# Performance work log

Measured on AMD Instinct MI355X. Metric: run time of the kernel, lower is better.

Reference implementation:

```python
import jax, jax.numpy as jnp
import numpy as np
from jax import lax

# Paraformer-large streaming decoder dims
L, H, DFF, NH, DK, K, V, T, S, CKV, LB = 16, 512, 2048, 4, 128, 11, 8404, 64, 2048, 256, 256


def _ln(x, g, b, eps=1e-5):
    m = jnp.mean(x, axis=-1, keepdims=True)
    var = jnp.mean((x - m) ** 2, axis=-1, keepdims=True)
    return (x - m) * lax.rsqrt(var + eps) * g + b


def setup_inputs() -> dict:
    key = jax.random.key(0)
    ks = jax.random.split(key, 20)
    w = lambda k, shp: jax.random.normal(k, shp, jnp.float32) * 0.02
    return {
        "encoder_out": jax.random.normal(ks[0], (1, S, H), jnp.float32),
        "list_frame": jax.random.normal(ks[1], (1, T, H), jnp.float32),
        "fsmn_cache": jax.random.normal(ks[2], (L, 1, H, K - 1), jnp.float32),
        "key_cache": jax.random.normal(ks[3], (L, NH, DK, CKV), jnp.float32),
        "value_cache": jax.random.normal(ks[4], (L, NH, CKV, DK), jnp.float32),
        "norm1_g": jnp.ones((L, H)), "norm1_b": jnp.zeros((L, H)),
        "norm2_g": jnp.ones((L, H)), "norm2_b": jnp.zeros((L, H)),
        "norm3_g": jnp.ones((L, H)), "norm3_b": jnp.zeros((L, H)),
        "ffn_norm_g": jnp.ones((L, DFF)), "ffn_norm_b": jnp.zeros((L, DFF)),
        "w1": w(ks[5], (L, H, DFF)), "b1": jnp.zeros((L, DFF)),
        "w2": w(ks[6], (L, DFF, H)),  # bias-free in FunASR DecoderSANM
        "fsmn_w": w(ks[7], (L, H, K)),  # depthwise conv, groups=H, no bias
        "qw": w(ks[8], (L, H, H)), "qb": jnp.zeros((L, H)),
        "kvw": w(ks[9], (L, H, 2 * H)), "kvb": jnp.zeros((L, 2 * H)),
        "ow": w(ks[10], (L, H, H)), "ob": jnp.zeros((L, H)),
        "d3_norm1_g": jnp.ones((H,)), "d3_norm1_b": jnp.zeros((H,)),
        "d3_w1": w(ks[11], (H, DFF)), "d3_b1": jnp.zeros((DFF,)),
        "d3_ffn_norm_g": jnp.ones((DFF,)), "d3_ffn_norm_b": jnp.zeros((DFF,)),
        "d3_w2": w(ks[12], (DFF, H)),
        "after_norm_g": jnp.ones((H,)), "after_norm_b": jnp.zeros((H,)),
        "out_w": w(ks[13], (H, V)), "out_b": jnp.zeros((V,)),
        "list_frame_len": T,
    }


def reference(encoder_out, list_frame, fsmn_cache, key_cache, value_cache,
              norm1_g, norm1_b, norm2_g, norm2_b, norm3_g, norm3_b,
              ffn_norm_g, ffn_norm_b, w1, b1, w2, fsmn_w, qw, qb, kvw, kvb, ow, ob,
              d3_norm1_g, d3_norm1_b, d3_w1, d3_b1, d3_ffn_norm_g, d3_ffn_norm_b, d3_w2,
              after_norm_g, after_norm_b, out_w, out_b, list_frame_len):
    enc = encoder_out[0]  # [S, H]
    scale = DK ** -0.5

    def layer_fn(lf, p):
        (fc, kc, vc, n1g, n1b, n2g, n2b, n3g, n3b, fng, fnb,
         W1, B1, W2, FW, QW, QB, KVW, KVB, OW, OB) = p
        residual = lf
        y = _ln(lf, n1g, n1b)
        y = _ln(jax.nn.relu(y @ W1 + B1), fng, fnb) @ W2
        y = _ln(y, n2g, n2b)
        # cache concat; slice [look_back:] with look_back = -(K-1)-T keeps all K-1+T cols
        x_cat = jnp.concatenate([fc, jnp.swapaxes(y, 1, 2)], axis=-1)  # [1, H, K-1+T]
        conv = lax.conv_general_dilated(
            x_cat, FW[:, None, :], (1,), 'VALID',
            dimension_numbers=('NCH', 'OIH', 'NCH'), feature_group_count=H)  # [1, H, T]
        x = jnp.swapaxes(conv, 1, 2) + y + residual
        residual = x
        q = (_ln(x, n3g, n3b)[0] @ QW + QB).reshape(-1, NH, DK).transpose(1, 0, 2) * scale  # [h, T, dk]
        kv = enc @ KVW + KVB  # [S, 2H]
        k = kv[:, :H].reshape(-1, NH, DK).transpose(1, 2, 0)  # [h, dk, S]
        v = kv[:, H:].reshape(-1, NH, DK).transpose(1, 0, 2)  # [h, S, dk]
        k = jnp.concatenate([kc, k], axis=2)  # [h, dk, CKV+S]
        v = jnp.concatenate([vc, v], axis=1)  # [h, CKV+S, dk]
        attn = jax.nn.softmax(jnp.einsum('htd,hds->hts', q, k), axis=-1)
        ctx = jnp.einsum('hts,hsd->htd', attn, v).transpose(1, 0, 2).reshape(1, -1, H)
        lf = residual + ctx @ OW + OB
        return lf, (x_cat, k[:, :, -LB:], v[:, -LB:, :])

    layer_params = (fsmn_cache, key_cache, value_cache, norm1_g, norm1_b, norm2_g, norm2_b,
                    norm3_g, norm3_b, ffn_norm_g, ffn_norm_b, w1, b1, w2, fsmn_w,
                    qw, qb, kvw, kvb, ow, ob)
    lf, (save_fsmn, save_keys, save_values) = lax.scan(layer_fn, list_frame, layer_params)
    x = _ln(lf, d3_norm1_g, d3_norm1_b)
    x = _ln(jax.nn.relu(x @ d3_w1 + d3_b1), d3_ffn_norm_g, d3_ffn_norm_b) @ d3_w2
    logits = _ln(x, after_norm_g, after_norm_b) @ out_w + out_b
    max_logit_ids = jnp.argmax(logits, axis=-1).astype(jnp.int32)
    return save_fsmn, save_keys, save_values, max_logit_ids
```

## Files before the change

kernel.cpp:

```cpp
#include <hip/hip_runtime.h>

constexpr int LAY = 16, HID = 512, FF = 2048, NHD = 4, DKH = 128, KW = 11,
              VOC = 8404, TT = 64, SEQ = 2048, LBN = 256;

__global__ void diag_k(float* __restrict__ p, float v) { p[threadIdx.x] = v; }

__global__ __launch_bounds__(256) void redln_k(
    const float* __restrict__ P, int N, int nch,
    const float* __restrict__ bias, const float* __restrict__ res, int relu,
    const float* __restrict__ g, const float* __restrict__ b,
    float* __restrict__ out1, float* __restrict__ out2) {
  __shared__ float buf[2048];
  __shared__ float red[256];
  const int m = blockIdx.x, tid = threadIdx.x;
  float s = 0.f;
  for (int n = tid; n < N; n += 256) {
    const float* p = P + (size_t)m * N + n;
    float v = 0.f;
    for (int c = 0; c < nch; ++c) v += p[(size_t)c * 64 * N];
    if (bias) v += bias[n];
    if (res) v += res[(size_t)m * N + n];
    if (relu) v = fmaxf(v, 0.f);
    if (out1) out1[(size_t)m * N + n] = v;
    buf[n] = v; s += v;
  }
  red[tid] = s; __syncthreads();
  for (int st = 128; st > 0; st >>= 1) { if (tid < st) red[tid] += red[tid + st]; __syncthreads(); }
  const float mean = red[0] / N;
  __syncthreads();
  float vs = 0.f;
  for (int n = tid; n < N; n += 256) { float d = buf[n] - mean; vs += d * d; }
  red[tid] = vs; __syncthreads();
  for (int st = 128; st > 0; st >>= 1) { if (tid < st) red[tid] += red[tid + st]; __syncthreads(); }
  const float inv = rsqrtf(red[0] / N + 1e-5f);
  for (int n = tid; n < N; n += 256)
    out2[(size_t)m * N + n] = (buf[n] - mean) * inv * g[n] + b[n];
}

__global__ __launch_bounds__(256) void gemm_nn(
    const float* __restrict__ A, int lda, long sA,
    const float* __restrict__ B, int ldb, long sB,
    float* __restrict__ C, int ldc, long sC,
    const float* __restrict__ bias,
    const float* __restrict__ res, int ldres,
    int N, int Kd, int flags, int nch,
    float* __restrict__ part, long pzs, int coff,
    int aCh, long aChS) {
  __shared__ float As[64][68];
  __shared__ float Bs[64][68];
  const int tid = threadIdx.x;
  const int lr = tid >> 4, lc = tid & 15;
  const int bn = blockIdx.x * 64;
  const int chunk = blockIdx.y;
  const int z = blockIdx.z;
  A += (long)z * sA; B += (long)z * sB; C += (long)z * sC;
  float acc[4][4] = {};
  const int ktiles = Kd >> 6;
  for (int kt = chunk; kt < ktiles; kt += nch) {
    const int k0 = kt << 6;
    __syncthreads();
#pragma unroll
    for (int i = 0; i < 4; ++i) {
      const int r = lr + 16 * i;
      const float* ap = A + (size_t)r * lda + k0 + lc * 4;
      float4 av = *(const float4*)ap;
      for (int c = 1; c < aCh; ++c) {
        const float4 t2 = *(const float4*)(ap + (size_t)c * aChS);
        av.x += t2.x; av.y += t2.y; av.z += t2.z; av.w += t2.w;
      }
      As[lc * 4 + 0][r] = av.x; As[lc * 4 + 1][r] = av.y;
      As[lc * 4 + 2][r] = av.z; As[lc * 4 + 3][r] = av.w;
      const int n = bn + lc * 4;
      const float* bp = B + (size_t)(k0 + r) * ldb + n;
      float4 bv;
      if (n + 3 < N) bv = *(const float4*)bp;
      else {
        bv.x = (n + 0 < N) ? bp[0] : 0.f;
        bv.y = (n + 1 < N) ? bp[1] : 0.f;
        bv.z = (n + 2 < N) ? bp[2] : 0.f;
        bv.w = (n + 3 < N) ? bp[3] : 0.f;
      }
      *(float4*)(&Bs[r][lc * 4]) = bv;
    }
    __syncthreads();
#pragma unroll 8
    for (int kk = 0; kk < 64; ++kk) {
      const float4 a = *(const float4*)(&As[kk][lr * 4]);
      const float4 b = *(const float4*)(&Bs[kk][lc * 4]);
      acc[0][0] += a.x * b.x; acc[0][1] += a.x * b.y; acc[0][2] += a.x * b.z; acc[0][3] += a.x * b.w;
      acc[1][0] += a.y * b.x; acc[1][1] += a.y * b.y; acc[1][2] += a.y * b.z; acc[1][3] += a.y * b.w;
      acc[2][0] += a.z * b.x; acc[2][1] += a.z * b.y; acc[2][2] += a.z * b.z; acc[2][3] += a.z * b.w;
      acc[3][0] += a.w * b.x; acc[3][1] += a.w * b.y; acc[3][2] += a.w * b.z; acc[3][3] += a.w * b.w;
    }
  }
  if (part) {
    float* P = part + (size_t)z * pzs + (size_t)(coff + chunk) * 64 * N;
#pragma unroll
    for (int i = 0; i < 4; ++i) {
      const int m = lr * 4 + i;
#pragma unroll
      for (int j = 0; j < 4; ++j) P[(size_t)m * N + bn + lc * 4 + j] = acc[i][j];
    }
    return;
  }
#pragma unroll
  for (int i = 0; i < 4; ++i) {
    const int m = lr * 4 + i;
#pragma unroll
    for (int j = 0; j < 4; ++j) {
      const int n = bn + lc * 4 + j;
      if (n < N) {
        float v = acc[i][j];
        if (bias) v += bias[n];
        if (res) v += res[(size_t)m * ldres + n];
        if (flags & 2) v += C[(size_t)m * ldc + n];
        if (flags & 1) v = fmaxf(v, 0.f);
        C[(size_t)m * ldc + n] = v;
      }
    }
  }
}

__global__ __launch_bounds__(256) void red_k(
    const float* __restrict__ P, float* __restrict__ out,
    int N, int nch, long pzs, int outld, int zoff,
    const float* __restrict__ bias, const float* __restrict__ res,
    const float* __restrict__ rsv, const float* __restrict__ bvv,
    int relu, int total) {
  const int idx = blockIdx.x * 256 + threadIdx.x;
  if (idx >= total) return;
  const int z = idx / (64 * N);
  const int rem = idx - z * 64 * N;
  const int t = rem / N;
  const int n = rem - t * N;
  const float* p = P + (size_t)z * pzs + (size_t)t * N + n;
  float s = 0.f;
  for (int c = 0; c < nch; ++c) s += p[(size_t)c * 64 * N];
  const int oc = z * zoff + n;
  if (bias) s += bias[oc];
  if (res) s += res[(size_t)t * outld + oc];
  if (rsv) s += rsv[z * 64 + t] * bvv[oc];
  if (relu) s = fmaxf(s, 0.f);
  out[(size_t)t * outld + oc] = s;
}

__global__ __launch_bounds__(256) void gemm_nt(
    const float* __restrict__ A, int lda, long sA,
    const float* __restrict__ B, int ldb, long sB,
    float* __restrict__ C, int ldc, long sC,
    int N, int Kd) {
  __shared__ float As[64][68];
  __shared__ float Bs[64][68];
  const int tid = threadIdx.x;
  const int lr = tid >> 4, lc = tid & 15;
  const int bn = blockIdx.x * 64;
  const int z = blockIdx.z;
  A += (long)z * sA; B += (long)z * sB; C += (long)z * sC;
  float acc[4][4] = {};
  for (int k0 = 0; k0 < Kd; k0 += 64) {
    __syncthreads();
#pragma unroll
    for (int i = 0; i < 4; ++i) {
      const int r = lr + 16 * i;
      const float4 av = *(const float4*)(A + (size_t)r * lda + k0 + lc * 4);
      As[lc * 4 + 0][r] = av.x; As[lc * 4 + 1][r] = av.y;
      As[lc * 4 + 2][r] = av.z; As[lc * 4 + 3][r] = av.w;
      const float4 bv = *(const float4*)(B + (size_t)(bn + r) * ldb + k0 + lc * 4);
      Bs[lc * 4 + 0][r] = bv.x; Bs[lc * 4 + 1][r] = bv.y;
      Bs[lc * 4 + 2][r] = bv.z; Bs[lc * 4 + 3][r] = bv.w;
    }
    __syncthreads();
#pragma unroll 8
    for (int kk = 0; kk < 64; ++kk) {
      const float4 a = *(const float4*)(&As[kk][lr * 4]);
      const float4 b = *(const float4*)(&Bs[kk][lc * 4]);
      acc[0][0] += a.x * b.x; acc[0][1] += a.x * b.y; acc[0][2] += a.x * b.z; acc[0][3] += a.x * b.w;
      acc[1][0] += a.y * b.x; acc[1][1] += a.y * b.y; acc[1][2] += a.y * b.z; acc[1][3] += a.y * b.w;
      acc[2][0] += a.z * b.x; acc[2][1] += a.z * b.y; acc[2][2] += a.z * b.z; acc[2][3] += a.z * b.w;
      acc[3][0] += a.w * b.x; acc[3][1] += a.w * b.y; acc[3][2] += a.w * b.z; acc[3][3] += a.w * b.w;
    }
  }
#pragma unroll
  for (int i = 0; i < 4; ++i) {
    const int m = lr * 4 + i;
#pragma unroll
    for (int j = 0; j < 4; ++j) {
      const int n = bn + lc * 4 + j;
      C[(size_t)m * ldc + n] = acc[i][j];
    }
  }
}

__global__ __launch_bounds__(256) void attn1_k(
    const float* __restrict__ qbf, const float* __restrict__ Wkv,
    const float* __restrict__ kcl,
    float* __restrict__ qp, float* __restrict__ sc,
    int ckv, int sct) {
  __shared__ float As[64][68];
  __shared__ float Bs[64][68];
  const int tid = threadIdx.x;
  const int lr = tid >> 4, lc = tid & 15;
  const int h = blockIdx.z;
  const bool isQp = blockIdx.x < 8;
  const int bn = (isQp ? blockIdx.x : blockIdx.x - 8) * 64;
  const float* A = qbf + h * DKH;
  float acc[4][4] = {};
  for (int k0 = 0; k0 < DKH; k0 += 64) {
    __syncthreads();
#pragma unroll
    for (int i = 0; i < 4; ++i) {
      const int r = lr + 16 * i;
      const float4 av = *(const float4*)(A + (size_t)r * HID + k0 + lc * 4);
      As[lc * 4 + 0][r] = av.x; As[lc * 4 + 1][r] = av.y;
      As[lc * 4 + 2][r] = av.z; As[lc * 4 + 3][r] = av.w;
      if (isQp) {
        const float4 bv = *(const float4*)(Wkv + (size_t)(bn + r) * (2 * HID) + h * DKH + k0 + lc * 4);
        Bs[lc * 4 + 0][r] = bv.x; Bs[lc * 4 + 1][r] = bv.y;
        Bs[lc * 4 + 2][r] = bv.z; Bs[lc * 4 + 3][r] = bv.w;
      } else {
        const float4 bv = *(const float4*)(kcl + ((size_t)h * DKH + k0 + r) * ckv + bn + lc * 4);
        *(float4*)(&Bs[r][lc * 4]) = bv;
      }
    }
    __syncthreads();
#pragma unroll 8
    for (int kk = 0; kk < 64; ++kk) {
      const float4 a = *(const float4*)(&As[kk][lr * 4]);
      const float4 b = *(const float4*)(&Bs[kk][lc * 4]);
      acc[0][0] += a.x * b.x; acc[0][1] += a.x * b.y; acc[0][2] += a.x * b.z; acc[0][3] += a.x * b.w;
      acc[1][0] += a.y * b.x; acc[1][1] += a.y * b.y; acc[1][2] += a.y * b.z; acc[1][3] += a.y * b.w;
      acc[2][0] += a.z * b.x; acc[2][1] += a.z * b.y; acc[2][2] += a.z * b.z; acc[2][3] += a.z * b.w;
      acc[3][0] += a.w * b.x; acc[3][1] += a.w * b.y; acc[3][2] += a.w * b.z; acc[3][3] += a.w * b.w;
    }
  }
  if (isQp) {
    float* C = qp + (size_t)h * TT * HID;
#pragma unroll
    for (int i = 0; i < 4; ++i)
#pragma unroll
      for (int j = 0; j < 4; ++j)
        C[(size_t)(lr * 4 + i) * HID + bn + lc * 4 + j] = acc[i][j];
  } else {
    float* C = sc + (size_t)h * TT * sct;
#pragma unroll
    for (int i = 0; i < 4; ++i)
#pragma unroll
      for (int j = 0; j < 4; ++j)
        C[(size_t)(lr * 4 + i) * sct + bn + lc * 4 + j] = acc[i][j];
  }
}

__global__ __launch_bounds__(256) void attn2_k(
    const float* __restrict__ sc, const float* __restrict__ vcl,
    const float* __restrict__ enc,
    float* __restrict__ part, float* __restrict__ partE,
    int ckv, int sct, int ncho, long pzc) {
  __shared__ float As[64][68];
  __shared__ float Bs[64][68];
  const int tid = threadIdx.x;
  const int lr = tid >> 4, lc = tid & 15;
  const int h = blockIdx.z;
  const int by = blockIdx.y;
  const bool isOld = blockIdx.x < 2;
  if (isOld && by >= ncho) return;
  if (!isOld && by >= 4) return;
  const float* A;
  const float* Bb;
  int lda, ldb, N, ktiles, nch, bn;
  float* P;
  if (isOld) {
    A = sc + (size_t)h * TT * sct;  lda = sct;
    Bb = vcl + (size_t)h * ckv * DKH; ldb = DKH;
    N = DKH; ktiles = ckv >> 6; nch = ncho; bn = blockIdx.x * 64;
    P = part + (size_t)h * pzc + (size_t)by * 64 * DKH;
  } else {
    A = sc + ckv + (size_t)h * TT * sct; lda = sct;
    Bb = enc; ldb = HID;
    N = HID; ktiles = SEQ >> 6; nch = 4; bn = (blockIdx.x - 2) * 64;
    P = partE + (size_t)h * (4L * 64 * HID) + (size_t)by * 64 * HID;
  }
  float acc[4][4] = {};
  for (int kt = by; kt < ktiles; kt += nch) {
    const int k0 = kt << 6;
    __syncthreads();
#pragma unroll
    for (int i = 0; i < 4; ++i) {
      const int r = lr + 16 * i;
      const float4 av = *(const float4*)(A + (size_t)r * lda + k0 + lc * 4);
      As[lc * 4 + 0][r] = av.x; As[lc * 4 + 1][r] = av.y;
      As[lc * 4 + 2][r] = av.z; As[lc * 4 + 3][r] = av.w;
      const float4 bv = *(const float4*)(Bb + (size_t)(k0 + r) * ldb + bn + lc * 4);
      *(float4*)(&Bs[r][lc * 4]) = bv;
    }
    __syncthreads();
#pragma unroll 8
    for (int kk = 0; kk < 64; ++kk) {
      const float4 a = *(const float4*)(&As[kk][lr * 4]);
      const float4 b = *(const float4*)(&Bs[kk][lc * 4]);
      acc[0][0] += a.x * b.x; acc[0][1] += a.x * b.y; acc[0][2] += a.x * b.z; acc[0][3] += a.x * b.w;
      acc[1][0] += a.y * b.x; acc[1][1] += a.y * b.y; acc[1][2] += a.y * b.z; acc[1][3] += a.y * b.w;
      acc[2][0] += a.z * b.x; acc[2][1] += a.z * b.y; acc[2][2] += a.z * b.z; acc[2][3] += a.z * b.w;
      acc[3][0] += a.w * b.x; acc[3][1] += a.w * b.y; acc[3][2] += a.w * b.z; acc[3][3] += a.w * b.w;
    }
  }
#pragma unroll
  for (int i = 0; i < 4; ++i)
#pragma unroll
    for (int j = 0; j < 4; ++j)
      P[(size_t)(lr * 4 + i) * N + bn + lc * 4 + j] = acc[i][j];
}

__global__ __launch_bounds__(128) void fsmn_k(const float* __restrict__ y4,
                                              const float* __restrict__ lfin,
                                              const float* __restrict__ cache,
                                              const float* __restrict__ fw,
                                              float* __restrict__ xout,
                                              float* __restrict__ xcat_out) {
  __shared__ float xc[KW - 1 + TT];
  const int tid = threadIdx.x, h = blockIdx.x;
  if (tid < KW - 1) xc[tid] = cache[h * (KW - 1) + tid];
  else if (tid < KW - 1 + TT) xc[tid] = y4[(size_t)(tid - (KW - 1)) * HID + h];
  __syncthreads();
  if (tid < KW - 1 + TT) xcat_out[h * (KW - 1 + TT) + tid] = xc[tid];
  if (tid < TT) {
    float a = 0.f;
#pragma unroll
    for (int k = 0; k < KW; ++k) a += xc[tid + k] * fw[h * KW + k];
    const size_t o = (size_t)tid * HID + h;
    xout[o] = a + y4[o] + lfin[o];
  }
}

__global__ __launch_bounds__(256) void softmax_k(float* __restrict__ sc,
                                                 float* __restrict__ rs,
                                                 const float* __restrict__ qbf,
                                                 const float* __restrict__ kb,
                                                 int cols, int newStart, float alpha) {
  __shared__ float red[256];
  const int tid = threadIdx.x;
  const int row = blockIdx.x;
  const int h = row >> 6, t = row & 63;
  sc += (size_t)row * cols;
  float qv = 0.f;
  if (tid < DKH) qv = qbf[t * HID + h * DKH + tid] * kb[h * DKH + tid];
  red[tid] = qv; __syncthreads();
  for (int st = 64; st > 0; st >>= 1) { if (tid < st) red[tid] += red[tid + st]; __syncthreads(); }
  const float qcv = red[0];
  __syncthreads();
  float m = -3.4e38f;
  for (int c = tid; c < cols; c += 256) {
    float v = (sc[c] + (c >= newStart ? qcv : 0.f)) * alpha;
    m = fmaxf(m, v);
  }
  red[tid] = m; __syncthreads();
  for (int st = 128; st > 0; st >>= 1) { if (tid < st) red[tid] = fmaxf(red[tid], red[tid + st]); __syncthreads(); }
  m = red[0]; __syncthreads();
  float s = 0.f;
  for (int c = tid; c < cols; c += 256) {
    float v = (sc[c] + (c >= newStart ? qcv : 0.f)) * alpha;
    float e = __expf(v - m);
    sc[c] = e; s += e;
  }
  red[tid] = s; __syncthreads();
  for (int st = 128; st > 0; st >>= 1) { if (tid < st) red[tid] += red[tid + st]; __syncthreads(); }
  const float inv = 1.f / red[0];
  float ns = 0.f;
  for (int c = tid; c < cols; c += 256) {
    float p = sc[c] * inv; sc[c] = p;
    if (c >= newStart) ns += p;
  }
  __syncthreads();
  red[tid] = ns; __syncthreads();
  for (int st = 128; st > 0; st >>= 1) { if (tid < st) red[tid] += red[tid + st]; __syncthreads(); }
  if (tid == 0) rs[row] = red[0];
}

__global__ __launch_bounds__(256) void argmax_k(const float* __restrict__ lg,
                                                float* __restrict__ out) {
  __shared__ float vs[256];
  __shared__ int ix[256];
  const int tid = threadIdx.x;
  lg += (size_t)blockIdx.x * VOC;
  float bm = -3.4e38f;
  int bi = 0;
  for (int c = tid; c < VOC; c += 256) { float v = lg[c]; if (v > bm) { bm = v; bi = c; } }
  vs[tid] = bm; ix[tid] = bi; __syncthreads();
  for (int st = 128; st > 0; st >>= 1) {
    if (tid < st) {
      if (vs[tid + st] > vs[tid] || (vs[tid + st] == vs[tid] && ix[tid + st] < ix[tid])) {
        vs[tid] = vs[tid + st]; ix[tid] = ix[tid + st];
      }
    }
    __syncthreads();
  }
  if (tid == 0) out[blockIdx.x] = (float)ix[0];
}

__global__ __launch_bounds__(256) void kvsave_k(const float* __restrict__ enc,
                                                const float* __restrict__ kvw,
                                                const float* __restrict__ kvb,
                                                float* __restrict__ keys,
                                                float* __restrict__ vals) {
  __shared__ float As[64][68];
  __shared__ float Bs[64][68];
  const int tid = threadIdx.x;
  const int lr = tid >> 4, lc = tid & 15;
  const int bn = blockIdx.x * 64, bm = blockIdx.y * 64;
  const int l = blockIdx.z;
  const float* W = kvw + (size_t)l * HID * 2 * HID;
  float acc[4][4] = {};
  for (int k0 = 0; k0 < HID; k0 += 64) {
    __syncthreads();
#pragma unroll
    for (int i = 0; i < 4; ++i) {
      const int r = lr + 16 * i;
      const float4 av =
          *(const float4*)(enc + (size_t)(SEQ - LBN + bm + r) * HID + k0 + lc * 4);
      As[lc * 4 + 0][r] = av.x; As[lc * 4 + 1][r] = av.y;
      As[lc * 4 + 2][r] = av.z; As[lc * 4 + 3][r] = av.w;
      const float4 bv = *(const float4*)(W + (size_t)(k0 + r) * (2 * HID) + bn + lc * 4);
      *(float4*)(&Bs[r][lc * 4]) = bv;
    }
    __syncthreads();
#pragma unroll 8
    for (int kk = 0; kk < 64; ++kk) {
      const float4 a = *(const float4*)(&As[kk][lr * 4]);
      const float4 b = *(const float4*)(&Bs[kk][lc * 4]);
      acc[0][0] += a.x * b.x; acc[0][1] += a.x * b.y; acc[0][2] += a.x * b.z; acc[0][3] += a.x * b.w;
      acc[1][0] += a.y * b.x; acc[1][1] += a.y * b.y; acc[1][2] += a.y * b.z; acc[1][3] += a.y * b.w;
      acc[2][0] += a.z * b.x; acc[2][1] += a.z * b.y; acc[2][2] += a.z * b.z; acc[2][3] += a.z * b.w;
      acc[3][0] += a.w * b.x; acc[3][1] += a.w * b.y; acc[3][2] += a.w * b.z; acc[3][3] += a.w * b.w;
    }
  }
#pragma unroll
  for (int i = 0; i < 4; ++i) {
    const int m = bm + lr * 4 + i;
#pragma unroll
    for (int j = 0; j < 4; ++j) {
      const int n = bn + lc * 4 + j;
      const float v = acc[i][j] + kvb[(size_t)l * 2 * HID + n];
      if (n < 512) {
        const int h = n >> 7, d = n & 127;
        keys[(((size_t)l * NHD + h) * DKH + d) * LBN + m] = v;
      } else {
        const int c = n - 512, h = c >> 7, d = c & 127;
        vals[(((size_t)l * NHD + h) * LBN + m) * DKH + d] = v;
      }
    }
  }
}

extern "C" void kernel_launch(void* const* d_in, const int* in_sizes, int n_in,
                              void* d_out, int out_size, void* d_ws, size_t ws_size,
                              hipStream_t stream) {
  static const int EXPECT[34] = {
      1048576, 32768, 81920, -1, -1,
      8192, 8192, 8192, 8192, 8192, 8192,
      32768, 32768,
      16777216, 32768, 16777216, 90112,
      4194304, 8192, 8388608, 16384, 4194304, 8192,
      512, 512, 1048576, 2048, 2048, 2048, 1048576,
      512, 512, 4302848, 8404};
  if (out_size != 4800576) {
    diag_k<<<1, 64, 0, stream>>>((float*)d_out, 9800000.f);
    return;
  }
  float* out_fsmn = (float*)d_out;
  float* out_keys = out_fsmn + (size_t)LAY * HID * (KW - 1 + TT);
  float* out_vals = out_keys + (size_t)LAY * NHD * DKH * LBN;
  float* out_ids  = out_vals + (size_t)LAY * NHD * LBN * DKH;
  if (n_in < 34) {
    diag_k<<<1, 64, 0, stream>>>(out_ids, 9900000.f);
    return;
  }
  for (int i = 0; i < 34; ++i) {
    if (EXPECT[i] >= 0 && in_sizes[i] != EXPECT[i]) {
      diag_k<<<1, 64, 0, stream>>>(out_ids, (float)((i + 1) * 100000));
      return;
    }
  }
  const long per = (long)LAY * NHD * DKH;
  const long ckl = (long)in_sizes[3] / per;
  if ((long)in_sizes[3] != ckl * per || in_sizes[4] != in_sizes[3] ||
      ckl <= 0 || (ckl & 63) != 0 || ckl > 6144) {
    diag_k<<<1, 64, 0, stream>>>(out_fsmn, (float)in_sizes[3]);
    return;
  }
  const int ckv = (int)ckl;
  const int sct = ckv + SEQ;
  const long TS = (long)TT * sct;
  const int ncho = (ckv / 64 < 8) ? (ckv / 64) : 8;

  const float* enc    = (const float*)d_in[0];
  const float* lfrm   = (const float*)d_in[1];
  const float* fcache = (const float*)d_in[2];
  const float* kcache = (const float*)d_in[3];
  const float* vcache = (const float*)d_in[4];
  const float* n1g = (const float*)d_in[5];  const float* n1b = (const float*)d_in[6];
  const float* n2g = (const float*)d_in[7];  const float* n2b = (const float*)d_in[8];
  const float* n3g = (const float*)d_in[9];  const float* n3b = (const float*)d_in[10];
  const float* fng = (const float*)d_in[11]; const float* fnb = (const float*)d_in[12];
  const float* w1  = (const float*)d_in[13]; const float* b1  = (const float*)d_in[14];
  const float* w2  = (const float*)d_in[15];
  const float* fw  = (const float*)d_in[16];
  const float* qw  = (const float*)d_in[17]; const float* qbi  = (const float*)d_in[18];
  const float* kvw = (const float*)d_in[19]; const float* kvbi = (const float*)d_in[20];
  const float* ow  = (const float*)d_in[21]; const float* obi  = (const float*)d_in[22];
  const float* d3n1g = (const float*)d_in[23]; const float* d3n1b = (const float*)d_in[24];
  const float* d3w1  = (const float*)d_in[25]; const float* d3b1  = (const float*)d_in[26];
  const float* d3fng = (const float*)d_in[27]; const float* d3fnb = (const float*)d_in[28];
  const float* d3w2  = (const float*)d_in[29];
  const float* ang   = (const float*)d_in[30]; const float* anb = (const float*)d_in[31];
  const float* outw  = (const float*)d_in[32]; const float* outb = (const float*)d_in[33];

  float* sc  = out_keys;
  float* ov  = out_vals;
  float* lf  = ov + 0;
  float* y1  = ov + 32768;
  float* y4  = ov + 98304;
  float* xb  = ov + 131072;
  float* qbf = ov + 163840;
  float* ctx = ov + 196608;
  float* y2  = ov + 360448;
  float* qp  = ov + 491520;
  float* rs  = ov + 753920;
  float* lg  = ov + 754176;
  float* partE = lg;
  float* part  = ov + 1292032;

  const float alpha = 0.08838834764831845f;
  const long TH = (long)TT * HID;
  const long pz_ctx = (long)(ncho + 4) * 64 * DKH;

  redln_k<<<TT, 256, 0, stream>>>(lfrm, HID, 1, nullptr, nullptr, 0,
                                  n1g, n1b, lf, y1);

  for (int l = 0; l < LAY; ++l) {
    const float* Wkv = kvw + (size_t)l * HID * 2 * HID;
    const float* Bkv = kvbi + (size_t)l * 2 * HID;
    gemm_nn<<<dim3(32, 4, 1), 256, 0, stream>>>(
        y1, HID, 0, w1 + (size_t)l * HID * FF, FF, 0, nullptr, 0, 0,
        nullptr, nullptr, 0, FF, HID, 0, 4, part, 0, 0, 1, 0);
    redln_k<<<TT, 256, 0, stream>>>(part, FF, 4, b1 + (size_t)l * FF, nullptr, 1,
                                    fng + (size_t)l * FF, fnb + (size_t)l * FF,
                                    nullptr, y2);
    gemm_nn<<<dim3(8, 16, 1), 256, 0, stream>>>(
        y2, FF, 0, w2 + (size_t)l * FF * HID, HID, 0, nullptr, 0, 0,
        nullptr, nullptr, 0, HID, FF, 0, 16, part, 0, 0, 1, 0);
    redln_k<<<TT, 256, 0, stream>>>(part, HID, 16, nullptr, nullptr, 0,
                                    n2g + l * HID, n2b + l * HID, nullptr, y4);
    fsmn_k<<<HID, 128, 0, stream>>>(y4, lf, fcache + (size_t)l * HID * (KW - 1),
                                    fw + (size_t)l * HID * KW, xb,
                                    out_fsmn + (size_t)l * HID * (KW - 1 + TT));
    redln_k<<<TT, 256, 0, stream>>>(xb, HID, 1, nullptr, nullptr, 0,
                                    n3g + l * HID, n3b + l * HID, nullptr, y1);
    gemm_nn<<<dim3(8, 8, 1), 256, 0, stream>>>(
        y1, HID, 0, qw + (size_t)l * HID * HID, HID, 0, nullptr, 0, 0,
        nullptr, nullptr, 0, HID, HID, 0, 8, part, 0, 0, 1, 0);
    red_k<<<128, 256, 0, stream>>>(part, qbf, HID, 8, 0, HID, HID,
                                   qbi + (size_t)l * HID, nullptr, nullptr, nullptr,
                                   0, TT * HID);
    attn1_k<<<dim3(8 + ckv / 64, 1, NHD), 256, 0, stream>>>(
        qbf, Wkv, kcache + (size_t)l * NHD * DKH * ckv, qp, sc, ckv, sct);
    gemm_nt<<<dim3(32, 1, NHD), 256, 0, stream>>>(
        qp, HID, TH, enc, HID, 0, sc + ckv, sct, TS, SEQ, HID);
    softmax_k<<<NHD * TT, 256, 0, stream>>>(sc, rs, qbf, Bkv, sct, ckv, alpha);
    attn2_k<<<dim3(10, (ncho > 4 ? ncho : 4), NHD), 256, 0, stream>>>(
        sc, vcache + (size_t)l * NHD * ckv * DKH, enc, part, partE,
        ckv, sct, ncho, pz_ctx);
    gemm_nn<<<dim3(2, 4, NHD), 256, 0, stream>>>(
        partE, HID, 4L * 64 * HID, Wkv + HID, 2 * HID, DKH, nullptr, 0, 0,
        nullptr, nullptr, 0, DKH, HID, 0, 4, part, pz_ctx, ncho, 4, 64L * HID);
    red_k<<<128, 256, 0, stream>>>(part, ctx, DKH, ncho + 4, pz_ctx, HID, DKH,
                                   nullptr, nullptr, rs, Bkv + HID, 0, NHD * TT * DKH);
    gemm_nn<<<dim3(8, 8, 1), 256, 0, stream>>>(
        ctx, HID, 0, ow + (size_t)l * HID * HID, HID, 0, nullptr, 0, 0,
        nullptr, nullptr, 0, HID, HID, 0, 8, part, 0, 0, 1, 0);
    const float* ng = (l + 1 < LAY) ? n1g + (l + 1) * HID : d3n1g;
    const float* nb = (l + 1 < LAY) ? n1b + (l + 1) * HID : d3n1b;
    redln_k<<<TT, 256, 0, stream>>>(part, HID, 8, obi + (size_t)l * HID, xb, 0,
                                    ng, nb, lf, y1);
  }

  gemm_nn<<<dim3(32, 4, 1), 256, 0, stream>>>(
      y1, HID, 0, d3w1, FF, 0, nullptr, 0, 0, nullptr, nullptr, 0,
      FF, HID, 0, 4, part, 0, 0, 1, 0);
  redln_k<<<TT, 256, 0, stream>>>(part, FF, 4, d3b1, nullptr, 1,
                                  d3fng, d3fnb, nullptr, y2);
  gemm_nn<<<dim3(8, 16, 1), 256, 0, stream>>>(
      y2, FF, 0, d3w2, HID, 0, nullptr, 0, 0, nullptr, nullptr, 0,
      HID, FF, 0, 16, part, 0, 0, 1, 0);
  redln_k<<<TT, 256, 0, stream>>>(part, HID, 16, nullptr, nullptr, 0,
                                  ang, anb, nullptr, y4);
  gemm_nn<<<dim3((VOC + 63) / 64, 1, 1), 256, 0, stream>>>(
      y4, HID, 0, outw, VOC, 0, lg, VOC, 0, outb, nullptr, 0,
      VOC, HID, 0, 1, nullptr, 0, 0, 1, 0);
  argmax_k<<<TT, 256, 0, stream>>>(lg, out_ids);

  kvsave_k<<<dim3(2 * HID / 64, LBN / 64, LAY), 256, 0, stream>>>(
      enc, kvw, kvbi, out_keys, out_vals);
}
```

Baseline: 2.985 ms.

## Swizzle shared tiles, raise split-K, fuse FSMN+LN and q reduction into consumers

Replaces padded 64x68 shared tiles with XOR-swizzled 64x64 layouts across all GEMM kernels to avoid bank conflicts. Doubles split-K chunk counts for FFN and attention GEMMs and adds split-K to gemm_nt, with partials moved to the workspace. Fuses the FSMN conv with the following LayerNorm, and folds the q-projection partial reduction into attn1 and softmax, removing a red_k launch. Softmax caches its row in shared memory so it no longer rereads global scores. More partial chunks add reduction traffic, and a workspace-size check is added.

```diff
diff --git a/kernel.cpp b/kernel.cpp
--- a/kernel.cpp
+++ b/kernel.cpp
@@ -2,6 +2,8 @@
 
 constexpr int LAY = 16, HID = 512, FF = 2048, NHD = 4, DKH = 128, KW = 11,
               VOC = 8404, TT = 64, SEQ = 2048, LBN = 256;
+
+#define SWZ(row, e) ((e) ^ ((((row) >> 2) & 7) << 2))
 
 __global__ void diag_k(float* __restrict__ p, float v) { p[threadIdx.x] = v; }
 
@@ -46,8 +48,8 @@
     int N, int Kd, int flags, int nch,
     float* __restrict__ part, long pzs, int coff,
     int aCh, long aChS) {
-  __shared__ float As[64][68];
-  __shared__ float Bs[64][68];
+  __shared__ float As[64][64];
+  __shared__ float Bs[64][64];
   const int tid = threadIdx.x;
   const int lr = tid >> 4, lc = tid & 15;
   const int bn = blockIdx.x * 64;
@@ -56,6 +58,7 @@
   A += (long)z * sA; B += (long)z * sB; C += (long)z * sC;
   float acc[4][4] = {};
   const int ktiles = Kd >> 6;
+  const int fa = (lc & 7) << 2;
   for (int kt = chunk; kt < ktiles; kt += nch) {
     const int k0 = kt << 6;
     __syncthreads();
@@ -68,8 +71,8 @@
         const float4 t2 = *(const float4*)(ap + (size_t)c * aChS);
         av.x += t2.x; av.y += t2.y; av.z += t2.z; av.w += t2.w;
       }
-      As[lc * 4 + 0][r] = av.x; As[lc * 4 + 1][r] = av.y;
-      As[lc * 4 + 2][r] = av.z; As[lc * 4 + 3][r] = av.w;
+      As[lc * 4 + 0][r ^ fa] = av.x; As[lc * 4 + 1][r ^ fa] = av.y;
+      As[lc * 4 + 2][r ^ fa] = av.z; As[lc * 4 + 3][r ^ fa] = av.w;
       const int n = bn + lc * 4;
       const float* bp = B + (size_t)(k0 + r) * ldb + n;
       float4 bv;
@@ -80,13 +83,14 @@
         bv.z = (n + 2 < N) ? bp[2] : 0.f;
         bv.w = (n + 3 < N) ? bp[3] : 0.f;
       }
-      *(float4*)(&Bs[r][lc * 4]) = bv;
+      *(float4*)(&Bs[r][SWZ(r, lc * 4)]) = bv;
     }
     __syncthreads();
 #pragma unroll 8
     for (int kk = 0; kk < 64; ++kk) {
-      const float4 a = *(const float4*)(&As[kk][lr * 4]);
-      const float4 b = *(const float4*)(&Bs[kk][lc * 4]);
+      const int fk = ((kk >> 2) & 7) << 2;
+      const float4 a = *(const float4*)(&As[kk][(lr * 4) ^ fk]);
+      const float4 b = *(const float4*)(&Bs[kk][(lc * 4) ^ fk]);
       acc[0][0] += a.x * b.x; acc[0][1] += a.x * b.y; acc[0][2] += a.x * b.z; acc[0][3] += a.x * b.w;
       acc[1][0] += a.y * b.x; acc[1][1] += a.y * b.y; acc[1][2] += a.y * b.z; acc[1][3] += a.y * b.w;
       acc[2][0] += a.z * b.x; acc[2][1] += a.z * b.y; acc[2][2] += a.z * b.z; acc[2][3] += a.z * b.w;
@@ -148,85 +152,103 @@
     const float* __restrict__ A, int lda, long sA,
     const float* __restrict__ B, int ldb, long sB,
     float* __restrict__ C, int ldc, long sC,
-    int N, int Kd) {
-  __shared__ float As[64][68];
-  __shared__ float Bs[64][68];
+    int N, int Kd, int nch, float* __restrict__ part) {
+  __shared__ float As[64][64];
+  __shared__ float Bs[64][64];
   const int tid = threadIdx.x;
   const int lr = tid >> 4, lc = tid & 15;
   const int bn = blockIdx.x * 64;
+  const int chunk = blockIdx.y;
   const int z = blockIdx.z;
   A += (long)z * sA; B += (long)z * sB; C += (long)z * sC;
   float acc[4][4] = {};
-  for (int k0 = 0; k0 < Kd; k0 += 64) {
+  const int ktiles = Kd >> 6;
+  const int fa = (lc & 7) << 2;
+  for (int kt = chunk; kt < ktiles; kt += nch) {
+    const int k0 = kt << 6;
     __syncthreads();
 #pragma unroll
     for (int i = 0; i < 4; ++i) {
       const int r = lr + 16 * i;
       const float4 av = *(const float4*)(A + (size_t)r * lda + k0 + lc * 4);
-      As[lc * 4 + 0][r] = av.x; As[lc * 4 + 1][r] = av.y;
-      As[lc * 4 + 2][r] = av.z; As[lc * 4 + 3][r] = av.w;
+      As[lc * 4 + 0][r ^ fa] = av.x; As[lc * 4 + 1][r ^ fa] = av.y;
+      As[lc * 4 + 2][r ^ fa] = av.z; As[lc * 4 + 3][r ^ fa] = av.w;
       const float4 bv = *(const float4*)(B + (size_t)(bn + r) * ldb + k0 + lc * 4);
-      Bs[lc * 4 + 0][r] = bv.x; Bs[lc * 4 + 1][r] = bv.y;
-      Bs[lc * 4 + 2][r] = bv.z; Bs[lc * 4 + 3][r] = bv.w;
+      Bs[lc * 4 + 0][r ^ fa] = bv.x; Bs[lc * 4 + 1][r ^ fa] = bv.y;
+      Bs[lc * 4 + 2][r ^ fa] = bv.z; Bs[lc * 4 + 3][r ^ fa] = bv.w;
     }
     __syncthreads();
 #pragma unroll 8
     for (int kk = 0; kk < 64; ++kk) {
-      const float4 a = *(const float4*)(&As[kk][lr * 4]);
-      const float4 b = *(const float4*)(&Bs[kk][lc * 4]);
+      const int fk = ((kk >> 2) & 7) << 2;
+      const float4 a = *(const float4*)(&As[kk][(lr * 4) ^ fk]);
+      const float4 b = *(const float4*)(&Bs[kk][(lc * 4) ^ fk]);
       acc[0][0] += a.x * b.x; acc[0][1] += a.x * b.y; acc[0][2] += a.x * b.z; acc[0][3] += a.x * b.w;
       acc[1][0] += a.y * b.x; acc[1][1] += a.y * b.y; acc[1][2] += a.y * b.z; acc[1][3] += a.y * b.w;
       acc[2][0] += a.z * b.x; acc[2][1] += a.z * b.y; acc[2][2] += a.z * b.z; acc[2][3] += a.z * b.w;
       acc[3][0] += a.w * b.x; acc[3][1] += a.w * b.y; acc[3][2] += a.w * b.z; acc[3][3] += a.w * b.w;
     }
   }
-#pragma unroll
-  for (int i = 0; i < 4; ++i) {
-    const int m = lr * 4 + i;
-#pragma unroll
-    for (int j = 0; j < 4; ++j) {
-      const int n = bn + lc * 4 + j;
-      C[(size_t)m * ldc + n] = acc[i][j];
-    }
+  if (chunk == 0) {
+#pragma unroll
+    for (int i = 0; i < 4; ++i)
+#pragma unroll
+      for (int j = 0; j < 4; ++j)
+        C[(size_t)(lr * 4 + i) * ldc + bn + lc * 4 + j] = acc[i][j];
+  } else {
+    float* P = part + (size_t)z * (64L * SEQ) + (size_t)(chunk - 1) * 64 * SEQ * NHD;
+#pragma unroll
+    for (int i = 0; i < 4; ++i)
+#pragma unroll
+      for (int j = 0; j < 4; ++j)
+        P[(size_t)(lr * 4 + i) * SEQ + bn + lc * 4 + j] = acc[i][j];
   }
 }
 
 __global__ __launch_bounds__(256) void attn1_k(
-    const float* __restrict__ qbf, const float* __restrict__ Wkv,
-    const float* __restrict__ kcl,
+    const float* __restrict__ qpart, const float* __restrict__ qbi_l,
+    const float* __restrict__ Wkv, const float* __restrict__ kcl,
     float* __restrict__ qp, float* __restrict__ sc,
     int ckv, int sct) {
-  __shared__ float As[64][68];
-  __shared__ float Bs[64][68];
+  __shared__ float As[64][64];
+  __shared__ float Bs[64][64];
   const int tid = threadIdx.x;
   const int lr = tid >> 4, lc = tid & 15;
   const int h = blockIdx.z;
   const bool isQp = blockIdx.x < 8;
   const int bn = (isQp ? blockIdx.x : blockIdx.x - 8) * 64;
-  const float* A = qbf + h * DKH;
+  const int fa = (lc & 7) << 2;
   float acc[4][4] = {};
   for (int k0 = 0; k0 < DKH; k0 += 64) {
     __syncthreads();
 #pragma unroll
     for (int i = 0; i < 4; ++i) {
       const int r = lr + 16 * i;
-      const float4 av = *(const float4*)(A + (size_t)r * HID + k0 + lc * 4);
-      As[lc * 4 + 0][r] = av.x; As[lc * 4 + 1][r] = av.y;
-      As[lc * 4 + 2][r] = av.z; As[lc * 4 + 3][r] = av.w;
+      const float* ap = qpart + (size_t)r * HID + h * DKH + k0 + lc * 4;
+      float4 av = *(const float4*)ap;
+      for (int c = 1; c < 8; ++c) {
+        const float4 t2 = *(const float4*)(ap + (size_t)c * 64 * HID);
+        av.x += t2.x; av.y += t2.y; av.z += t2.z; av.w += t2.w;
+      }
+      const float4 bb = *(const float4*)(qbi_l + h * DKH + k0 + lc * 4);
+      av.x += bb.x; av.y += bb.y; av.z += bb.z; av.w += bb.w;
+      As[lc * 4 + 0][r ^ fa] = av.x; As[lc * 4 + 1][r ^ fa] = av.y;
+      As[lc * 4 + 2][r ^ fa] = av.z; As[lc * 4 + 3][r ^ fa] = av.w;
       if (isQp) {
         const float4 bv = *(const float4*)(Wkv + (size_t)(bn + r) * (2 * HID) + h * DKH + k0 + lc * 4);
-        Bs[lc * 4 + 0][r] = bv.x; Bs[lc * 4 + 1][r] = bv.y;
-        Bs[lc * 4 + 2][r] = bv.z; Bs[lc * 4 + 3][r] = bv.w;
+        Bs[lc * 4 + 0][r ^ fa] = bv.x; Bs[lc * 4 + 1][r ^ fa] = bv.y;
+        Bs[lc * 4 + 2][r ^ fa] = bv.z; Bs[lc * 4 + 3][r ^ fa] = bv.w;
       } else {
         const float4 bv = *(const float4*)(kcl + ((size_t)h * DKH + k0 + r) * ckv + bn + lc * 4);
-        *(float4*)(&Bs[r][lc * 4]) = bv;
+        *(float4*)(&Bs[r][SWZ(r, lc * 4)]) = bv;
       }
     }
     __syncthreads();
 #pragma unroll 8
     for (int kk = 0; kk < 64; ++kk) {
-      const float4 a = *(const float4*)(&As[kk][lr * 4]);
-      const float4 b = *(const float4*)(&Bs[kk][lc * 4]);
+      const int fk = ((kk >> 2) & 7) << 2;
+      const float4 a = *(const float4*)(&As[kk][(lr * 4) ^ fk]);
+      const float4 b = *(const float4*)(&Bs[kk][(lc * 4) ^ fk]);
       acc[0][0] += a.x * b.x; acc[0][1] += a.x * b.y; acc[0][2] += a.x * b.z; acc[0][3] += a.x * b.w;
       acc[1][0] += a.y * b.x; acc[1][1] += a.y * b.y; acc[1][2] += a.y * b.z; acc[1][3] += a.y * b.w;
       acc[2][0] += a.z * b.x; acc[2][1] += a.z * b.y; acc[2][2] += a.z * b.z; acc[2][3] += a.z * b.w;
@@ -255,15 +277,15 @@
     const float* __restrict__ enc,
     float* __restrict__ part, float* __restrict__ partE,
     int ckv, int sct, int ncho, long pzc) {
-  __shared__ float As[64][68];
-  __shared__ float Bs[64][68];
+  __shared__ float As[64][64];
+  __shared__ float Bs[64][64];
   const int tid = threadIdx.x;
   const int lr = tid >> 4, lc = tid & 15;
   const int h = blockIdx.z;
   const int by = blockIdx.y;
   const bool isOld = blockIdx.x < 2;
   if (isOld && by >= ncho) return;
-  if (!isOld && by >= 4) return;
+  if (!isOld && by >= 8) return;
   const float* A;
   const float* Bb;
   int lda, ldb, N, ktiles, nch, bn;
@@ -276,9 +298,10 @@
   } else {
     A = sc + ckv + (size_t)h * TT * sct; lda = sct;
     Bb = enc; ldb = HID;
-    N = HID; ktiles = SEQ >> 6; nch = 4; bn = (blockIdx.x - 2) * 64;
-    P = partE + (size_t)h * (4L * 64 * HID) + (size_t)by * 64 * HID;
-  }
+    N = HID; ktiles = SEQ >> 6; nch = 8; bn = (blockIdx.x - 2) * 64;
+    P = partE + (size_t)h * (8L * 64 * HID) + (size_t)by * 64 * HID;
+  }
+  const int fa = (lc & 7) << 2;
   float acc[4][4] = {};
   for (int kt = by; kt < ktiles; kt += nch) {
     const int k0 = kt << 6;
@@ -287,16 +310,17 @@
     for (int i = 0; i < 4; ++i) {
       const int r = lr + 16 * i;
       const float4 av = *(const float4*)(A + (size_t)r * lda + k0 + lc * 4);
-      As[lc * 4 + 0][r] = av.x; As[lc * 4 + 1][r] = av.y;
-      As[lc * 4 + 2][r] = av.z; As[lc * 4 + 3][r] = av.w;
+      As[lc * 4 + 0][r ^ fa] = av.x; As[lc * 4 + 1][r ^ fa] = av.y;
+      As[lc * 4 + 2][r ^ fa] = av.z; As[lc * 4 + 3][r ^ fa] = av.w;
       const float4 bv = *(const float4*)(Bb + (size_t)(k0 + r) * ldb + bn + lc * 4);
-      *(float4*)(&Bs[r][lc * 4]) = bv;
+      *(float4*)(&Bs[r][SWZ(r, lc * 4)]) = bv;
     }
     __syncthreads();
 #pragma unroll 8
     for (int kk = 0; kk < 64; ++kk) {
-      const float4 a = *(const float4*)(&As[kk][lr * 4]);
-      const float4 b = *(const float4*)(&Bs[kk][lc * 4]);
+      const int fk = ((kk >> 2) & 7) << 2;
+      const float4 a = *(const float4*)(&As[kk][(lr * 4) ^ fk]);
+      const float4 b = *(const float4*)(&Bs[kk][(lc * 4) ^ fk]);
       acc[0][0] += a.x * b.x; acc[0][1] += a.x * b.y; acc[0][2] += a.x * b.z; acc[0][3] += a.x * b.w;
       acc[1][0] += a.y * b.x; acc[1][1] += a.y * b.y; acc[1][2] += a.y * b.z; acc[1][3] += a.y * b.w;
       acc[2][0] += a.z * b.x; acc[2][1] += a.z * b.y; acc[2][2] += a.z * b.z; acc[2][3] += a.z * b.w;
@@ -310,63 +334,93 @@
       P[(size_t)(lr * 4 + i) * N + bn + lc * 4 + j] = acc[i][j];
 }
 
-__global__ __launch_bounds__(128) void fsmn_k(const float* __restrict__ y4,
-                                              const float* __restrict__ lfin,
-                                              const float* __restrict__ cache,
-                                              const float* __restrict__ fw,
-                                              float* __restrict__ xout,
-                                              float* __restrict__ xcat_out) {
-  __shared__ float xc[KW - 1 + TT];
-  const int tid = threadIdx.x, h = blockIdx.x;
-  if (tid < KW - 1) xc[tid] = cache[h * (KW - 1) + tid];
-  else if (tid < KW - 1 + TT) xc[tid] = y4[(size_t)(tid - (KW - 1)) * HID + h];
+__global__ __launch_bounds__(256) void fsmnln_k(
+    const float* __restrict__ y4, const float* __restrict__ lfin,
+    const float* __restrict__ cache, const float* __restrict__ fw,
+    const float* __restrict__ g, const float* __restrict__ b,
+    float* __restrict__ xb, float* __restrict__ xcat,
+    float* __restrict__ y1out) {
+  __shared__ float buf[HID];
+  __shared__ float red[256];
+  const int t = blockIdx.x, tid = threadIdx.x;
+  float s = 0.f;
+  for (int h = tid; h < HID; h += 256) {
+    float conv = 0.f;
+#pragma unroll
+    for (int k = 0; k < KW; ++k) {
+      const int j = t + k;
+      const float xcv = (j < KW - 1) ? cache[h * (KW - 1) + j]
+                                     : y4[(size_t)(j - (KW - 1)) * HID + h];
+      conv += xcv * fw[h * KW + k];
+    }
+    const float yv = y4[(size_t)t * HID + h];
+    const float x = conv + yv + lfin[(size_t)t * HID + h];
+    xb[(size_t)t * HID + h] = x;
+    buf[h] = x; s += x;
+    xcat[h * (KW - 1 + TT) + (KW - 1) + t] = yv;
+    if (t == 0) {
+      for (int j2 = 0; j2 < KW - 1; ++j2)
+        xcat[h * (KW - 1 + TT) + j2] = cache[h * (KW - 1) + j2];
+    }
+  }
+  red[tid] = s; __syncthreads();
+  for (int st = 128; st > 0; st >>= 1) { if (tid < st) red[tid] += red[tid + st]; __syncthreads(); }
+  const float mean = red[0] / HID;
   __syncthreads();
-  if (tid < KW - 1 + TT) xcat_out[h * (KW - 1 + TT) + tid] = xc[tid];
-  if (tid < TT) {
-    float a = 0.f;
-#pragma unroll
-    for (int k = 0; k < KW; ++k) a += xc[tid + k] * fw[h * KW + k];
-    const size_t o = (size_t)tid * HID + h;
-    xout[o] = a + y4[o] + lfin[o];
-  }
-}
-
-__global__ __launch_bounds__(256) void softmax_k(float* __restrict__ sc,
-                                                 float* __restrict__ rs,
-                                                 const float* __restrict__ qbf,
-                                                 const float* __restrict__ kb,
-                                                 int cols, int newStart, float alpha) {
+  float vs = 0.f;
+  for (int h = tid; h < HID; h += 256) { float d = buf[h] - mean; vs += d * d; }
+  red[tid] = vs; __syncthreads();
+  for (int st = 128; st > 0; st >>= 1) { if (tid < st) red[tid] += red[tid + st]; __syncthreads(); }
+  const float inv = rsqrtf(red[0] / HID + 1e-5f);
+  for (int h = tid; h < HID; h += 256)
+    y1out[(size_t)t * HID + h] = (buf[h] - mean) * inv * g[h] + b[h];
+}
+
+__global__ __launch_bounds__(256) void softmax_k(
+    float* __restrict__ sc, float* __restrict__ rs,
+    const float* __restrict__ qpart, const float* __restrict__ qbi_l,
+    const float* __restrict__ kb, const float* __restrict__ partN,
+    int cols, int newStart, float alpha) {
+  __shared__ float srow[8192];
   __shared__ float red[256];
   const int tid = threadIdx.x;
   const int row = blockIdx.x;
   const int h = row >> 6, t = row & 63;
   sc += (size_t)row * cols;
+  const float* pn = partN + (size_t)h * 64 * SEQ + (size_t)t * SEQ;
   float qv = 0.f;
-  if (tid < DKH) qv = qbf[t * HID + h * DKH + tid] * kb[h * DKH + tid];
+  if (tid < DKH) {
+    const float* qp0 = qpart + (size_t)t * HID + h * DKH + tid;
+    float q = qp0[0];
+    for (int c = 1; c < 8; ++c) q += qp0[(size_t)c * 64 * HID];
+    q += qbi_l[h * DKH + tid];
+    qv = q * kb[h * DKH + tid];
+  }
   red[tid] = qv; __syncthreads();
   for (int st = 64; st > 0; st >>= 1) { if (tid < st) red[tid] += red[tid + st]; __syncthreads(); }
   const float qcv = red[0];
   __syncthreads();
   float m = -3.4e38f;
   for (int c = tid; c < cols; c += 256) {
-    float v = (sc[c] + (c >= newStart ? qcv : 0.f)) * alpha;
-    m = fmaxf(m, v);
+    float v = sc[c];
+    if (c >= newStart) v += pn[c - newStart] + qcv;
+    v *= alpha;
+    srow[c] = v; m = fmaxf(m, v);
   }
   red[tid] = m; __syncthreads();
   for (int st = 128; st > 0; st >>= 1) { if (tid < st) red[tid] = fmaxf(red[tid], red[tid + st]); __syncthreads(); }
   m = red[0]; __syncthreads();
   float s = 0.f;
   for (int c = tid; c < cols; c += 256) {
-    float v = (sc[c] + (c >= newStart ? qcv : 0.f)) * alpha;
-    float e = __expf(v - m);
-    sc[c] = e; s += e;
+    const float e = __expf(srow[c] - m);
+    srow[c] = e; s += e;
   }
   red[tid] = s; __syncthreads();
   for (int st = 128; st > 0; st >>= 1) { if (tid < st) red[tid] += red[tid + st]; __syncthreads(); }
   const float inv = 1.f / red[0];
   float ns = 0.f;
   for (int c = tid; c < cols; c += 256) {
-    float p = sc[c] * inv; sc[c] = p;
+    const float p = srow[c] * inv; sc[c] = p;
     if (c >= newStart) ns += p;
   }
   __syncthreads();
@@ -401,13 +455,14 @@
                                                 const float* __restrict__ kvb,
                                                 float* __restrict__ keys,
                                                 float* __restrict__ vals) {
-  __shared__ float As[64][68];
-  __shared__ float Bs[64][68];
+  __shared__ float As[64][64];
+  __shared__ float Bs[64][64];
   const int tid = threadIdx.x;
   const int lr = tid >> 4, lc = tid & 15;
   const int bn = blockIdx.x * 64, bm = blockIdx.y * 64;
   const int l = blockIdx.z;
   const float* W = kvw + (size_t)l * HID * 2 * HID;
+  const int fa = (lc & 7) << 2;
   float acc[4][4] = {};
   for (int k0 = 0; k0 < HID; k0 += 64) {
     __syncthreads();
@@ -416,16 +471,17 @@
       const int r = lr + 16 * i;
       const float4 av =
           *(const float4*)(enc + (size_t)(SEQ - LBN + bm + r) * HID + k0 + lc * 4);
-      As[lc * 4 + 0][r] = av.x; As[lc * 4 + 1][r] = av.y;
-      As[lc * 4 + 2][r] = av.z; As[lc * 4 + 3][r] = av.w;
+      As[lc * 4 + 0][r ^ fa] = av.x; As[lc * 4 + 1][r ^ fa] = av.y;
+      As[lc * 4 + 2][r ^ fa] = av.z; As[lc * 4 + 3][r ^ fa] = av.w;
       const float4 bv = *(const float4*)(W + (size_t)(k0 + r) * (2 * HID) + bn + lc * 4);
-      *(float4*)(&Bs[r][lc * 4]) = bv;
+      *(float4*)(&Bs[r][SWZ(r, lc * 4)]) = bv;
     }
     __syncthreads();
 #pragma unroll 8
     for (int kk = 0; kk < 64; ++kk) {
-      const float4 a = *(const float4*)(&As[kk][lr * 4]);
-      const float4 b = *(const float4*)(&Bs[kk][lc * 4]);
+      const int fk = ((kk >> 2) & 7) << 2;
+      const float4 a = *(const float4*)(&As[kk][(lr * 4) ^ fk]);
+      const float4 b = *(const float4*)(&Bs[kk][(lc * 4) ^ fk]);
       acc[0][0] += a.x * b.x; acc[0][1] += a.x * b.y; acc[0][2] += a.x * b.z; acc[0][3] += a.x * b.w;
       acc[1][0] += a.y * b.x; acc[1][1] += a.y * b.y; acc[1][2] += a.y * b.z; acc[1][3] += a.y * b.w;
       acc[2][0] += a.z * b.x; acc[2][1] += a.z * b.y; acc[2][2] += a.z * b.z; acc[2][3] += a.z * b.w;
@@ -484,6 +540,10 @@
   if ((long)in_sizes[3] != ckl * per || in_sizes[4] != in_sizes[3] ||
       ckl <= 0 || (ckl & 63) != 0 || ckl > 6144) {
     diag_k<<<1, 64, 0, stream>>>(out_fsmn, (float)in_sizes[3]);
+    return;
+  }
+  if (ws_size < (size_t)3145728 * 4) {
+    diag_k<<<1, 64, 0, stream>>>(out_fsmn, 1.0e6f + (float)(ws_size >> 20));
     return;
   }
   const int ckv = (int)ckl;
@@ -519,14 +579,15 @@
   float* y1  = ov + 32768;
   float* y4  = ov + 98304;
   float* xb  = ov + 131072;
-  float* qbf = ov + 163840;
   float* ctx = ov + 196608;
   float* y2  = ov + 360448;
   float* qp  = ov + 491520;
   float* rs  = ov + 753920;
   float* lg  = ov + 754176;
-  float* partE = lg;
-  float* part  = ov + 1292032;
+  float* wsf   = (float*)d_ws;
+  float* part  = wsf;
+  float* partE = wsf + 1048576;
+  float* partN = wsf + 2097152;
 
   const float alpha = 0.08838834764831845f;
   const long TH = (long)TT * HID;
@@ -538,39 +599,37 @@
   for (int l = 0; l < LAY; ++l) {
     const float* Wkv = kvw + (size_t)l * HID * 2 * HID;
     const float* Bkv = kvbi + (size_t)l * 2 * HID;
-    gemm_nn<<<dim3(32, 4, 1), 256, 0, stream>>>(
+    const float* qbi_l = qbi + (size_t)l * HID;
+    gemm_nn<<<dim3(32, 8, 1), 256, 0, stream>>>(
         y1, HID, 0, w1 + (size_t)l * HID * FF, FF, 0, nullptr, 0, 0,
-        nullptr, nullptr, 0, FF, HID, 0, 4, part, 0, 0, 1, 0);
-    redln_k<<<TT, 256, 0, stream>>>(part, FF, 4, b1 + (size_t)l * FF, nullptr, 1,
+        nullptr, nullptr, 0, FF, HID, 0, 8, part, 0, 0, 1, 0);
+    redln_k<<<TT, 256, 0, stream>>>(part, FF, 8, b1 + (size_t)l * FF, nullptr, 1,
                                     fng + (size_t)l * FF, fnb + (size_t)l * FF,
                                     nullptr, y2);
-    gemm_nn<<<dim3(8, 16, 1), 256, 0, stream>>>(
+    gemm_nn<<<dim3(8, 32, 1), 256, 0, stream>>>(
         y2, FF, 0, w2 + (size_t)l * FF * HID, HID, 0, nullptr, 0, 0,
-        nullptr, nullptr, 0, HID, FF, 0, 16, part, 0, 0, 1, 0);
-    redln_k<<<TT, 256, 0, stream>>>(part, HID, 16, nullptr, nullptr, 0,
+        nullptr, nullptr, 0, HID, FF, 0, 32, part, 0, 0, 1, 0);
+    redln_k<<<TT, 256, 0, stream>>>(part, HID, 32, nullptr, nullptr, 0,
                                     n2g + l * HID, n2b + l * HID, nullptr, y4);
-    fsmn_k<<<HID, 128, 0, stream>>>(y4, lf, fcache + (size_t)l * HID * (KW - 1),
-                                    fw + (size_t)l * HID * KW, xb,
-                                    out_fsmn + (size_t)l * HID * (KW - 1 + TT));
-    redln_k<<<TT, 256, 0, stream>>>(xb, HID, 1, nullptr, nullptr, 0,
-                                    n3g + l * HID, n3b + l * HID, nullptr, y1);
+    fsmnln_k<<<TT, 256, 0, stream>>>(y4, lf, fcache + (size_t)l * HID * (KW - 1),
+                                     fw + (size_t)l * HID * KW,
+                                     n3g + l * HID, n3b + l * HID,
+                                     xb, out_fsmn + (size_t)l * HID * (KW - 1 + TT), y1);
     gemm_nn<<<dim3(8, 8, 1), 256, 0, stream>>>(
         y1, HID, 0, qw + (size_t)l * HID * HID, HID, 0, nullptr, 0, 0,
         nullptr, nullptr, 0, HID, HID, 0, 8, part, 0, 0, 1, 0);
-    red_k<<<128, 256, 0, stream>>>(part, qbf, HID, 8, 0, HID, HID,
-                                   qbi + (size_t)l * HID, nullptr, nullptr, nullptr,
-                                   0, TT * HID);
     attn1_k<<<dim3(8 + ckv / 64, 1, NHD), 256, 0, stream>>>(
-        qbf, Wkv, kcache + (size_t)l * NHD * DKH * ckv, qp, sc, ckv, sct);
-    gemm_nt<<<dim3(32, 1, NHD), 256, 0, stream>>>(
-        qp, HID, TH, enc, HID, 0, sc + ckv, sct, TS, SEQ, HID);
-    softmax_k<<<NHD * TT, 256, 0, stream>>>(sc, rs, qbf, Bkv, sct, ckv, alpha);
-    attn2_k<<<dim3(10, (ncho > 4 ? ncho : 4), NHD), 256, 0, stream>>>(
+        part, qbi_l, Wkv, kcache + (size_t)l * NHD * DKH * ckv, qp, sc, ckv, sct);
+    gemm_nt<<<dim3(32, 2, NHD), 256, 0, stream>>>(
+        qp, HID, TH, enc, HID, 0, sc + ckv, sct, TS, SEQ, HID, 2, partN);
+    softmax_k<<<NHD * TT, 256, 0, stream>>>(sc, rs, part, qbi_l, Bkv, partN,
+                                            sct, ckv, alpha);
+    attn2_k<<<dim3(10, 8, NHD), 256, 0, stream>>>(
         sc, vcache + (size_t)l * NHD * ckv * DKH, enc, part, partE,
         ckv, sct, ncho, pz_ctx);
     gemm_nn<<<dim3(2, 4, NHD), 256, 0, stream>>>(
-        partE, HID, 4L * 64 * HID, Wkv + HID, 2 * HID, DKH, nullptr, 0, 0,
-        nullptr, nullptr, 0, DKH, HID, 0, 4, part, pz_ctx, ncho, 4, 64L * HID);
+        partE, HID, 8L * 64 * HID, Wkv + HID, 2 * HID, DKH, nullptr, 0, 0,
+        nullptr, nullptr, 0, DKH, HID, 0, 4, part, pz_ctx, ncho, 8, 64L * HID);
     red_k<<<128, 256, 0, stream>>>(part, ctx, DKH, ncho + 4, pz_ctx, HID, DKH,
                                    nullptr, nullptr, rs, Bkv + HID, 0, NHD * TT * DKH);
     gemm_nn<<<dim3(8, 8, 1), 256, 0, stream>>>(
@@ -582,15 +641,15 @@
                                     ng, nb, lf, y1);
   }
 
-  gemm_nn<<<dim3(32, 4, 1), 256, 0, stream>>>(
+  gemm_nn<<<dim3(32, 8, 1), 256, 0, stream>>>(
       y1, HID, 0, d3w1, FF, 0, nullptr, 0, 0, nullptr, nullptr, 0,
-      FF, HID, 0, 4, part, 0, 0, 1, 0);
-  redln_k<<<TT, 256, 0, stream>>>(part, FF, 4, d3b1, nullptr, 1,
+      FF, HID, 0, 8, part, 0, 0, 1, 0);
+  redln_k<<<TT, 256, 0, stream>>>(part, FF, 8, d3b1, nullptr, 1,
                                   d3fng, d3fnb, nullptr, y2);
-  gemm_nn<<<dim3(8, 16, 1), 256, 0, stream>>>(
+  gemm_nn<<<dim3(8, 32, 1), 256, 0, stream>>>(
       y2, FF, 0, d3w2, HID, 0, nullptr, 0, 0, nullptr, nullptr, 0,
-      HID, FF, 0, 16, part, 0, 0, 1, 0);
-  redln_k<<<TT, 256, 0, stream>>>(part, HID, 16, nullptr, nullptr, 0,
+      HID, FF, 0, 32, part, 0, 0, 1, 0);
+  redln_k<<<TT, 256, 0, stream>>>(part, HID, 32, nullptr, nullptr, 0,
                                   ang, anb, nullptr, y4);
   gemm_nn<<<dim3((VOC + 63) / 64, 1, 1), 256, 0, stream>>>(
       y4, HID, 0, outw, VOC, 0, lg, VOC, 0, outb, nullptr, 0,
```

Result: no change. 3.015 ms (+1.0%).
